# Kernel tuning notes

Measured on AMD Instinct MI355X. Metric: run time of the kernel, lower is better.

The kernel has to match this reference:

```python
import jax, jax.numpy as jnp
import numpy as np

H, N, CH, L = 256, 256, 1, 1024


def setup_inputs() -> dict:
    key = jax.random.key(0)
    k1, k2, k3, k4 = jax.random.split(key, 4)
    # Hurwitz-like A so the discretized dA is stable (|eig| < 1) over L powers
    A = 0.05 * jax.random.normal(k1, (H, N, N), jnp.float32) - jnp.eye(N, dtype=jnp.float32)
    B = jax.random.normal(k2, (H, N), jnp.float32)
    C = jax.random.normal(k3, (CH, H, N), jnp.float32)
    log_dt = jax.random.uniform(k4, (H,), jnp.float32,
                                minval=np.log(1e-3), maxval=np.log(1e-1))
    return {"A": A, "B": B, "C": C, "log_dt": log_dt}


def reference(A, B, C, log_dt):
    # Bilinear (Tustin) discretization:
    #   dA = (I - dt/2 A)^{-1} (I + dt/2 A),  dB = dt * (I - dt/2 A)^{-1} B
    dt = jnp.exp(log_dt)                                   # (H,)
    I = jnp.eye(A.shape[-1], dtype=A.dtype)
    A_bwd = I - (dt[:, None, None] / 2) * A                # (H, N, N)
    A_fwd = I + (dt[:, None, None] / 2) * A                # (H, N, N)
    dB = dt[:, None] * jnp.linalg.solve(A_bwd, B[..., None])[..., 0]   # (H, N)
    dA = jnp.linalg.solve(A_bwd, A_fwd)                    # (H, N, N)

    # Krylov kernel: k[c,h,l] = C[c,h,:] @ dA^l @ dB[h,:]
    def step(x, _):
        y = jnp.einsum('chn,hn->ch', C, x)                 # contract with C
        x_next = jnp.einsum('hmn,hn->hm', dA, x)           # advance state
        return x_next, y

    _, ys = jax.lax.scan(step, dB, None, length=L)         # ys: (L, CH, H)
    k = jnp.transpose(ys, (1, 2, 0))                       # (CH, H, L)
    return k
```

## Files before the change

### kernel.cpp

```cpp
#include <hip/hip_runtime.h>
#include <cstdint>
#include <cstddef>

#define NH 256
#define ND 256
#define NSV 32

typedef __attribute__((ext_vector_type(4))) float f32x4;
typedef __attribute__((ext_vector_type(8))) short short8;
typedef __attribute__((ext_vector_type(8))) unsigned short u16x8;
typedef __attribute__((ext_vector_type(4))) unsigned short u16x4;
typedef __attribute__((ext_vector_type(4))) unsigned int u32x4;

__device__ __forceinline__ float bfrec(unsigned short hi, unsigned short lo) {
  return __uint_as_float(((unsigned)hi) << 16) + __uint_as_float(((unsigned)lo) << 16);
}
__device__ __forceinline__ unsigned rne16(unsigned u) {
  return u + 0x7FFFu + ((u >> 16) & 1u);
}
__device__ __forceinline__ void bfsplit(float x, unsigned short& hi, unsigned short& lo) {
  unsigned u = __float_as_uint(x);
  unsigned r1 = rne16(u);
  hi = (unsigned short)(r1 >> 16);
  float lf = x - __uint_as_float(r1 & 0xFFFF0000u);
  unsigned r2 = rne16(__float_as_uint(lf));
  lo = (unsigned short)(r2 >> 16);
}
__device__ __forceinline__ void gload16(const void* g, void* l) {
  __builtin_amdgcn_global_load_lds(
      (const __attribute__((address_space(1))) unsigned int*)g,
      (__attribute__((address_space(3))) unsigned int*)l, 16, 0, 0);
}
__device__ __forceinline__ int ksw(int row) { return (row >> 1) & 3; }

__global__ __launch_bounds__(256) void prep_kernel(
    const float* __restrict__ A, const float* __restrict__ log_dt,
    unsigned short* __restrict__ Mhi, unsigned short* __restrict__ Mlo)
{
  size_t e0 = ((size_t)blockIdx.x * 256 + threadIdx.x) * 16;
  int h = (int)(e0 >> 16);
  float hdt = 0.5f * __expf(log_dt[h]);
  unsigned short hb[16], lb[16];
#pragma unroll
  for (int i = 0; i < 4; ++i) {
    f32x4 v = *(const f32x4*)(A + e0 + i * 4);
#pragma unroll
    for (int j = 0; j < 4; ++j) bfsplit(v[j] * hdt, hb[i * 4 + j], lb[i * 4 + j]);
  }
  unsigned ph[8], pl[8];
#pragma unroll
  for (int i = 0; i < 8; ++i) {
    ph[i] = (unsigned)hb[2 * i] | ((unsigned)hb[2 * i + 1] << 16);
    pl[i] = (unsigned)lb[2 * i] | ((unsigned)lb[2 * i + 1] << 16);
  }
  u32x4 a0 = {ph[0], ph[1], ph[2], ph[3]}, a1 = {ph[4], ph[5], ph[6], ph[7]};
  u32x4 b0 = {pl[0], pl[1], pl[2], pl[3]}, b1 = {pl[4], pl[5], pl[6], pl[7]};
  *(u32x4*)(Mhi + e0) = a0; *(u32x4*)(Mhi + e0 + 8) = a1;
  *(u32x4*)(Mlo + e0) = b0; *(u32x4*)(Mlo + e0 + 8) = b1;
}

template <int YI, int QOUT, int DBOUT>
__global__ __launch_bounds__(256) void gemm128_kernel(
    const unsigned short* __restrict__ Xhi, const unsigned short* __restrict__ Xlo,
    const unsigned short* __restrict__ Yhi, const unsigned short* __restrict__ Ylo,
    unsigned short* __restrict__ Dhi, unsigned short* __restrict__ Dlo,
    unsigned short* __restrict__ Qhi, unsigned short* __restrict__ Qlo,
    const float* __restrict__ Bv, float* __restrict__ dBraw)
{
  __shared__ unsigned short lds[33792];
  int tid = threadIdx.x;
  int lane = tid & 63, w = tid >> 6;
  int bid = blockIdx.x;
  int part = (bid >> 3) & 3;
  int h = ((bid >> 5) << 3) | (bid & 7);
  int m0 = (part >> 1) * 128, n0 = (part & 1) * 128;
  size_t mb = (size_t)h * 65536;

  f32x4 acc[2][8];
#pragma unroll
  for (int m = 0; m < 2; ++m)
#pragma unroll
    for (int n = 0; n < 8; ++n) { f32x4 z = {0.f, 0.f, 0.f, 0.f}; acc[m][n] = z; }

  auto STAGE = [&](int s, int kb) {
#pragma unroll
    for (int j = 0; j < 2; ++j) {
      int c = j * 256 + tid;
      {
        int row = c >> 2, sp = c & 3;
        size_t go = mb + (size_t)(m0 + row) * 256 + kb * 32 + ((sp ^ ksw(row)) << 3);
        gload16(Xhi + go, &lds[s * 8192 + c * 8]);
        gload16(Xlo + go, &lds[s * 8192 + 4096 + c * 8]);
      }
      {
        int k = c >> 4, ns = c & 15;
        size_t go = mb + (size_t)(kb * 32 + k) * 256 + n0 + ns * 8;
        gload16(Yhi + go, &lds[16384 + s * 8192 + c * 8]);
        gload16(Ylo + go, &lds[16384 + s * 8192 + 4096 + c * 8]);
      }
    }
  };

  STAGE(0, 0);
  __builtin_amdgcn_sched_barrier(0);

  int nn = tid & 127, kh = tid >> 7;
  int cur = 0;
  for (int kb = 0; kb < 8; ++kb) {
    int nxt = cur ^ 1;
    if (kb < 7) {
      STAGE(nxt, kb + 1);
      __builtin_amdgcn_sched_barrier(0);
      asm volatile("s_waitcnt vmcnt(8)" ::: "memory");
    } else {
      asm volatile("s_waitcnt vmcnt(0)" ::: "memory");
    }
    __builtin_amdgcn_sched_barrier(0);
    __builtin_amdgcn_s_barrier();
    __builtin_amdgcn_sched_barrier(0);

    unsigned short* yb = &lds[16384 + cur * 8192];
    unsigned short rh[16], rl[16];
#pragma unroll
    for (int i = 0; i < 16; ++i) {
      rh[i] = yb[(kh * 16 + i) * 128 + nn];
      rl[i] = yb[4096 + (kh * 16 + i) * 128 + nn];
    }
    asm volatile("s_waitcnt lgkmcnt(0)" ::: "memory");
    __builtin_amdgcn_sched_barrier(0);
    __builtin_amdgcn_s_barrier();
    __builtin_amdgcn_sched_barrier(0);

#pragma unroll
    for (int s2 = 0; s2 < 2; ++s2) {
      int sl = kh * 2 + s2;
      int off = nn * 32 + ((sl ^ ksw(nn)) << 3);
      u16x8 vh, vl;
#pragma unroll
      for (int e = 0; e < 8; ++e) {
        unsigned short hh = rh[s2 * 8 + e], ll = rl[s2 * 8 + e];
        if (YI) {
          if (kb * 32 + kh * 16 + s2 * 8 + e == n0 + nn) {
            float vv = bfrec(hh, ll) + 1.0f;
            bfsplit(vv, hh, ll);
          }
        }
        vh[e] = hh; vl[e] = ll;
      }
      *(u16x8*)&yb[off] = vh;
      *(u16x8*)&yb[4096 + off] = vl;
    }
    asm volatile("s_waitcnt lgkmcnt(0)" ::: "memory");
    __builtin_amdgcn_sched_barrier(0);
    __builtin_amdgcn_s_barrier();
    __builtin_amdgcn_sched_barrier(0);

    int kg = lane >> 4, li = lane & 15;
    const unsigned short* xb = &lds[cur * 8192];
    short8 bhi[8], blo[8];
#pragma unroll
    for (int n = 0; n < 8; ++n) {
      int rowN = n * 16 + li;
      int off = rowN * 32 + ((kg ^ ksw(rowN)) << 3);
      bhi[n] = *(const short8*)&yb[off];
      blo[n] = *(const short8*)&yb[4096 + off];
    }
    __builtin_amdgcn_s_setprio(1);
#pragma unroll
    for (int m = 0; m < 2; ++m) {
      int rowM = w * 32 + m * 16 + li;
      int off = rowM * 32 + ((kg ^ ksw(rowM)) << 3);
      short8 ahi = *(const short8*)&xb[off];
      short8 alo = *(const short8*)&xb[4096 + off];
#pragma unroll
      for (int n = 0; n < 8; ++n) {
        acc[m][n] = __builtin_amdgcn_mfma_f32_16x16x32_bf16(ahi, bhi[n], acc[m][n], 0, 0, 0);
        acc[m][n] = __builtin_amdgcn_mfma_f32_16x16x32_bf16(ahi, blo[n], acc[m][n], 0, 0, 0);
        acc[m][n] = __builtin_amdgcn_mfma_f32_16x16x32_bf16(alo, bhi[n], acc[m][n], 0, 0, 0);
      }
    }
    __builtin_amdgcn_s_setprio(0);
    __builtin_amdgcn_sched_barrier(0);
    __builtin_amdgcn_s_barrier();
    __builtin_amdgcn_sched_barrier(0);
    cur = nxt;
  }

  float* fb = (float*)lds;
  {
    int q0 = (lane >> 4) * 4, li = lane & 15;
#pragma unroll
    for (int m = 0; m < 2; ++m)
#pragma unroll
      for (int n = 0; n < 8; ++n)
#pragma unroll
        for (int q = 0; q < 4; ++q)
          fb[(w * 32 + m * 16 + q0 + q) * 132 + n * 16 + li] = acc[m][n][q];
  }
  __syncthreads();
  {
    int row = tid >> 1, half = tid & 1;
    float dacc = 0.f;
#pragma unroll 1
    for (int hp = 0; hp < 2; ++hp) {
      int c0 = half * 64 + hp * 32;
      float v[32];
#pragma unroll
      for (int u = 0; u < 8; ++u) {
        f32x4 t4 = *(const f32x4*)&fb[row * 132 + c0 + u * 4];
#pragma unroll
        for (int e = 0; e < 4; ++e) v[u * 4 + e] = t4[e];
      }
      size_t go = mb + (size_t)(m0 + row) * 256 + n0 + c0;
      if (DBOUT) {
        const float* Bp = Bv + h * 256 + n0 + c0;
#pragma unroll
        for (int u = 0; u < 8; ++u) {
          f32x4 b4 = *(const f32x4*)(Bp + u * 4);
#pragma unroll
          for (int e = 0; e < 4; ++e) dacc += v[u * 4 + e] * b4[e];
        }
      }
      {
        unsigned hw[16], lw[16];
#pragma unroll
        for (int i = 0; i < 16; ++i) {
          unsigned short ha, la, hb2, lb2;
          bfsplit(v[2 * i], ha, la);
          bfsplit(v[2 * i + 1], hb2, lb2);
          hw[i] = (unsigned)ha | ((unsigned)hb2 << 16);
          lw[i] = (unsigned)la | ((unsigned)lb2 << 16);
        }
#pragma unroll
        for (int u = 0; u < 4; ++u) {
          u32x4 a = {hw[u * 4], hw[u * 4 + 1], hw[u * 4 + 2], hw[u * 4 + 3]};
          u32x4 b = {lw[u * 4], lw[u * 4 + 1], lw[u * 4 + 2], lw[u * 4 + 3]};
          *(u32x4*)(Dhi + go + u * 8) = a;
          *(u32x4*)(Dlo + go + u * 8) = b;
        }
      }
      if (QOUT) {
        float xv[32];
#pragma unroll
        for (int u = 0; u < 4; ++u) {
          u16x8 xh = *(const u16x8*)(Xhi + go + u * 8);
          u16x8 xl = *(const u16x8*)(Xlo + go + u * 8);
#pragma unroll
          for (int e = 0; e < 8; ++e) xv[u * 8 + e] = bfrec(xh[e], xl[e]);
        }
        int grow = m0 + row, gc0 = n0 + c0;
        float qv[32];
#pragma unroll
        for (int e = 0; e < 32; ++e)
          qv[e] = v[e] + 2.f * xv[e] + ((gc0 + e) == grow ? 1.f : 0.f);
        unsigned hw[16], lw[16];
#pragma unroll
        for (int i = 0; i < 16; ++i) {
          unsigned short ha, la, hb2, lb2;
          bfsplit(qv[2 * i], ha, la);
          bfsplit(qv[2 * i + 1], hb2, lb2);
          hw[i] = (unsigned)ha | ((unsigned)hb2 << 16);
          lw[i] = (unsigned)la | ((unsigned)lb2 << 16);
        }
#pragma unroll
        for (int u = 0; u < 4; ++u) {
          u32x4 a = {hw[u * 4], hw[u * 4 + 1], hw[u * 4 + 2], hw[u * 4 + 3]};
          u32x4 b = {lw[u * 4], lw[u * 4 + 1], lw[u * 4 + 2], lw[u * 4 + 3]};
          *(u32x4*)(Qhi + go + u * 8) = a;
          *(u32x4*)(Qlo + go + u * 8) = b;
        }
      }
    }
    if (DBOUT) {
      int slab = (part & 1) * 2 + half;
      dBraw[(size_t)slab * 65536 + h * 256 + m0 + row] = dacc;
    }
  }
}

__device__ __forceinline__ int physc(int c) { return c + ((c >> 4) << 2); }

__global__ __launch_bounds__(1024, 4) void chain32_kernel(
    const unsigned short* __restrict__ dAhi, const unsigned short* __restrict__ dAlo,
    const unsigned short* __restrict__ Ghi, const unsigned short* __restrict__ Glo,
    const float* __restrict__ Cin, const float* __restrict__ Bv,
    const float* __restrict__ log_dt, const float* __restrict__ dBraw,
    float* __restrict__ U, float* __restrict__ W)
{
  int b = blockIdx.x;
  bool um = b < NH;
  int h = um ? b : b - NH;
  float* out = (um ? U : W) + (size_t)h * (NSV * 256);

  int tid = threadIdx.x;
  int rg = tid >> 4, cg = tid & 15;
  float mat[4][16];
  if (um) {
    const unsigned short* mh = dAhi + (size_t)h * 65536;
    const unsigned short* ml = dAlo + (size_t)h * 65536;
#pragma unroll
    for (int j = 0; j < 16; ++j) {
      u16x4 h4 = *(const u16x4*)(mh + (size_t)(cg * 16 + j) * 256 + rg * 4);
      u16x4 l4 = *(const u16x4*)(ml + (size_t)(cg * 16 + j) * 256 + rg * 4);
#pragma unroll
      for (int rr = 0; rr < 4; ++rr) mat[rr][j] = bfrec(h4[rr], l4[rr]);
    }
  } else {
    const unsigned short* mh = Ghi + (size_t)h * 65536;
    const unsigned short* ml = Glo + (size_t)h * 65536;
#pragma unroll
    for (int rr = 0; rr < 4; ++rr) {
      const unsigned short* ph = mh + (size_t)(rg * 4 + rr) * 256 + cg * 16;
      const unsigned short* pl = ml + (size_t)(rg * 4 + rr) * 256 + cg * 16;
      u16x8 h0 = *(const u16x8*)ph, h1 = *(const u16x8*)(ph + 8);
      u16x8 l0 = *(const u16x8*)pl, l1 = *(const u16x8*)(pl + 8);
#pragma unroll
      for (int e = 0; e < 8; ++e) {
        mat[rr][e] = bfrec(h0[e], l0[e]);
        mat[rr][8 + e] = bfrec(h1[e], l1[e]);
      }
    }
  }
  __shared__ float xb[2][320];
  __shared__ float slab[16][260];
  if (tid < 256) {
    float vv;
    if (um) {
      vv = Cin[(size_t)h * 256 + tid];
    } else {
      int o = h * 256 + tid;
      float raw = dBraw[o] + dBraw[65536 + o] + dBraw[131072 + o] + dBraw[196608 + o];
      vv = 0.5f * __expf(log_dt[h]) * (raw + Bv[o]);
    }
    xb[0][physc(tid)] = vv;
    out[tid] = vv;
  }
  __syncthreads();
  int p = 0;
  for (int v = 1; v < NSV; ++v) {
    f32x4 part = {0.f, 0.f, 0.f, 0.f};
#pragma unroll
    for (int sl = 0; sl < 4; ++sl) {
      f32x4 xv = *(const f32x4*)&xb[p][cg * 20 + sl * 4];
#pragma unroll
      for (int rr = 0; rr < 4; ++rr)
#pragma unroll
        for (int e = 0; e < 4; ++e) part[rr] += mat[rr][sl * 4 + e] * xv[e];
    }
    *(f32x4*)&slab[cg][rg * 4] = part;
    __syncthreads();
    if (tid < 256) {
      int row = tid;
      float s = 0.f;
#pragma unroll
      for (int c = 0; c < 16; ++c) s += slab[c][row];
      xb[p ^ 1][physc(row)] = s;
      out[(size_t)v * 256 + row] = s;
    }
    __syncthreads();
    p ^= 1;
  }
}

__global__ __launch_bounds__(512) void gram_kernel(
    const float* __restrict__ U, const float* __restrict__ W, float* __restrict__ out)
{
  int b = blockIdx.x;
  int h = b >> 1, jh = b & 1;
  __shared__ float ul[32][260];
  __shared__ float wl[16][260];
  int tid = threadIdx.x;
  const float* Up = U + (size_t)h * (NSV * 256);
  const float* Wp = W + (size_t)h * (NSV * 256) + (size_t)jh * 16 * 256;
  {
    int r = tid >> 4, cb = (tid & 15) * 16;
#pragma unroll
    for (int u = 0; u < 4; ++u) {
      f32x4 a = *(const f32x4*)(Up + (size_t)r * 256 + cb + u * 4);
      *(f32x4*)&ul[r][cb + u * 4] = a;
    }
  }
  {
    int r = tid >> 5, cb = (tid & 31) * 8;
    f32x4 a = *(const f32x4*)(Wp + (size_t)r * 256 + cb);
    f32x4 c2 = *(const f32x4*)(Wp + (size_t)r * 256 + cb + 4);
    *(f32x4*)&wl[r][cb] = a;
    *(f32x4*)&wl[r][cb + 4] = c2;
  }
  __syncthreads();
  int i = tid & 31, j2 = tid >> 5;
  float acc = 0.f;
#pragma unroll 8
  for (int c = 0; c < 256; c += 4) {
    f32x4 uu = *(const f32x4*)&ul[i][c];
    f32x4 ww = *(const f32x4*)&wl[j2][c];
    acc += uu[0] * ww[0] + uu[1] * ww[1] + uu[2] * ww[2] + uu[3] * ww[3];
  }
  out[(size_t)h * 1024 + (size_t)(jh * 16 + j2) * 32 + i] = acc;
}

__global__ void bail_kernel(float* out, unsigned mib) {
  if (threadIdx.x == 0) out[blockIdx.x] = -(2.0e6f + (float)mib * 4096.0f);
}

extern "C" void kernel_launch(void* const* d_in, const int* in_sizes, int n_in,
                              void* d_out, int out_size, void* d_ws, size_t ws_size,
                              hipStream_t stream) {
  const float* A = (const float*)d_in[0];
  const float* B = (const float*)d_in[1];
  const float* C = (const float*)d_in[2];
  const float* log_dt = (const float*)d_in[3];
  float* out = (float*)d_out;

  const size_t PLANE = (size_t)NH * ND * ND * 2;
  const size_t DBRAW = 4 * (size_t)NH * ND * 4;
  const size_t USZ = (size_t)NH * NSV * ND * 4;
  const size_t WSZ = USZ;
  const size_t NEED = 6 * PLANE + DBRAW + USZ + WSZ;
  if (ws_size < NEED) {
    bail_kernel<<<8, 64, 0, stream>>>(out, (unsigned)(ws_size >> 20));
    return;
  }
  uint8_t* w8 = (uint8_t*)d_ws;
  auto P = [&](int i) -> unsigned short* { return (unsigned short*)(w8 + (size_t)i * PLANE); };
  float* dBraw = (float*)(w8 + 6 * PLANE);
  float* Up = (float*)(w8 + 6 * PLANE + DBRAW);
  float* Wp = (float*)(w8 + 6 * PLANE + DBRAW + USZ);

  prep_kernel<<<4096, 256, 0, stream>>>(A, log_dt, P(0), P(1));
  gemm128_kernel<0, 1, 0><<<1024, 256, 0, stream>>>(P(0), P(1), P(0), P(1),
                                                    P(2), P(3), P(4), P(5), nullptr, nullptr);
  gemm128_kernel<1, 0, 0><<<1024, 256, 0, stream>>>(P(4), P(5), P(2), P(3),
                                                    P(0), P(1), nullptr, nullptr, nullptr, nullptr);
  gemm128_kernel<0, 0, 0><<<1024, 256, 0, stream>>>(P(2), P(3), P(2), P(3),
                                                    P(4), P(5), nullptr, nullptr, nullptr, nullptr);
  gemm128_kernel<1, 0, 1><<<1024, 256, 0, stream>>>(P(0), P(1), P(4), P(5),
                                                    P(2), P(3), nullptr, nullptr, B, dBraw);
  gemm128_kernel<0, 0, 0><<<1024, 256, 0, stream>>>(P(2), P(3), P(2), P(3),
                                                    P(0), P(1), nullptr, nullptr, nullptr, nullptr);
  gemm128_kernel<0, 0, 0><<<1024, 256, 0, stream>>>(P(0), P(1), P(0), P(1),
                                                    P(4), P(5), nullptr, nullptr, nullptr, nullptr);
  gemm128_kernel<0, 0, 0><<<1024, 256, 0, stream>>>(P(4), P(5), P(4), P(5),
                                                    P(0), P(1), nullptr, nullptr, nullptr, nullptr);
  gemm128_kernel<0, 0, 0><<<1024, 256, 0, stream>>>(P(0), P(1), P(0), P(1),
                                                    P(4), P(5), nullptr, nullptr, nullptr, nullptr);
  gemm128_kernel<0, 0, 0><<<1024, 256, 0, stream>>>(P(4), P(5), P(4), P(5),
                                                    P(0), P(1), nullptr, nullptr, nullptr, nullptr);
  chain32_kernel<<<2 * NH, 1024, 0, stream>>>(P(2), P(3), P(0), P(1),
                                              C, B, log_dt, dBraw, Up, Wp);
  gram_kernel<<<2 * NH, 512, 0, stream>>>(Up, Wp, out);
}
```

Measured before the change: 585.9 us.

## Use 512-thread blocks for 128x128 GEMM tiles with separate transposed-B LDS buffer

Doubles the GEMM workgroup from 256 to 512 threads so each wave computes a 16-row slice instead of 32, halving per-thread accumulators, staging loads and epilogue work. The B-transpose now writes to a dedicated LDS region, which removes one barrier per k-step. The epilogue splits each row across four threads, and the dB partial-sum slabs grow from 4 to 8, with the chain kernel summing all 8. The aim is more waves to hide latency, at the cost of more LDS per block, a 4-waves-per-SIMD register cap, and more dBraw workspace.

```diff
diff --git a/kernel.cpp b/kernel.cpp
--- a/kernel.cpp
+++ b/kernel.cpp
@@ -60,14 +60,14 @@
 }
 
 template <int YI, int QOUT, int DBOUT>
-__global__ __launch_bounds__(256) void gemm128_kernel(
+__global__ __launch_bounds__(512, 4) void gemm128_kernel(
     const unsigned short* __restrict__ Xhi, const unsigned short* __restrict__ Xlo,
     const unsigned short* __restrict__ Yhi, const unsigned short* __restrict__ Ylo,
     unsigned short* __restrict__ Dhi, unsigned short* __restrict__ Dlo,
     unsigned short* __restrict__ Qhi, unsigned short* __restrict__ Qlo,
     const float* __restrict__ Bv, float* __restrict__ dBraw)
 {
-  __shared__ unsigned short lds[33792];
+  __shared__ unsigned short lds[40960];
   int tid = threadIdx.x;
   int lane = tid & 63, w = tid >> 6;
   int bid = blockIdx.x;
@@ -76,28 +76,22 @@
   int m0 = (part >> 1) * 128, n0 = (part & 1) * 128;
   size_t mb = (size_t)h * 65536;
 
-  f32x4 acc[2][8];
-#pragma unroll
-  for (int m = 0; m < 2; ++m)
-#pragma unroll
-    for (int n = 0; n < 8; ++n) { f32x4 z = {0.f, 0.f, 0.f, 0.f}; acc[m][n] = z; }
+  f32x4 acc[8];
+#pragma unroll
+  for (int n = 0; n < 8; ++n) { f32x4 z = {0.f, 0.f, 0.f, 0.f}; acc[n] = z; }
 
   auto STAGE = [&](int s, int kb) {
-#pragma unroll
-    for (int j = 0; j < 2; ++j) {
-      int c = j * 256 + tid;
-      {
-        int row = c >> 2, sp = c & 3;
-        size_t go = mb + (size_t)(m0 + row) * 256 + kb * 32 + ((sp ^ ksw(row)) << 3);
-        gload16(Xhi + go, &lds[s * 8192 + c * 8]);
-        gload16(Xlo + go, &lds[s * 8192 + 4096 + c * 8]);
-      }
-      {
-        int k = c >> 4, ns = c & 15;
-        size_t go = mb + (size_t)(kb * 32 + k) * 256 + n0 + ns * 8;
-        gload16(Yhi + go, &lds[16384 + s * 8192 + c * 8]);
-        gload16(Ylo + go, &lds[16384 + s * 8192 + 4096 + c * 8]);
-      }
+    {
+      int row = tid >> 2, sp = tid & 3;
+      size_t go = mb + (size_t)(m0 + row) * 256 + kb * 32 + ((sp ^ ksw(row)) << 3);
+      gload16(Xhi + go, &lds[s * 8192 + tid * 8]);
+      gload16(Xlo + go, &lds[s * 8192 + 4096 + tid * 8]);
+    }
+    {
+      int k = tid >> 4, ns = tid & 15;
+      size_t go = mb + (size_t)(kb * 32 + k) * 256 + n0 + ns * 8;
+      gload16(Yhi + go, &lds[16384 + s * 8192 + tid * 8]);
+      gload16(Ylo + go, &lds[16384 + s * 8192 + 4096 + tid * 8]);
     }
   };
 
@@ -111,7 +105,7 @@
     if (kb < 7) {
       STAGE(nxt, kb + 1);
       __builtin_amdgcn_sched_barrier(0);
-      asm volatile("s_waitcnt vmcnt(8)" ::: "memory");
+      asm volatile("s_waitcnt vmcnt(4)" ::: "memory");
     } else {
       asm volatile("s_waitcnt vmcnt(0)" ::: "memory");
     }
@@ -119,67 +113,59 @@
     __builtin_amdgcn_s_barrier();
     __builtin_amdgcn_sched_barrier(0);
 
-    unsigned short* yb = &lds[16384 + cur * 8192];
-    unsigned short rh[16], rl[16];
-#pragma unroll
-    for (int i = 0; i < 16; ++i) {
-      rh[i] = yb[(kh * 16 + i) * 128 + nn];
-      rl[i] = yb[4096 + (kh * 16 + i) * 128 + nn];
-    }
-    asm volatile("s_waitcnt lgkmcnt(0)" ::: "memory");
-    __builtin_amdgcn_sched_barrier(0);
-    __builtin_amdgcn_s_barrier();
-    __builtin_amdgcn_sched_barrier(0);
-
-#pragma unroll
-    for (int s2 = 0; s2 < 2; ++s2) {
-      int sl = kh * 2 + s2;
-      int off = nn * 32 + ((sl ^ ksw(nn)) << 3);
+    {
+      const unsigned short* yb = &lds[16384 + cur * 8192];
+      unsigned short rh[8], rl[8];
+#pragma unroll
+      for (int i = 0; i < 8; ++i) {
+        rh[i] = yb[(kh * 8 + i) * 128 + nn];
+        rl[i] = yb[4096 + (kh * 8 + i) * 128 + nn];
+      }
+      int off = nn * 32 + ((kh ^ ksw(nn)) << 3);
       u16x8 vh, vl;
 #pragma unroll
       for (int e = 0; e < 8; ++e) {
-        unsigned short hh = rh[s2 * 8 + e], ll = rl[s2 * 8 + e];
+        unsigned short hh = rh[e], ll = rl[e];
         if (YI) {
-          if (kb * 32 + kh * 16 + s2 * 8 + e == n0 + nn) {
+          if (kb * 32 + kh * 8 + e == n0 + nn) {
             float vv = bfrec(hh, ll) + 1.0f;
             bfsplit(vv, hh, ll);
           }
         }
         vh[e] = hh; vl[e] = ll;
       }
-      *(u16x8*)&yb[off] = vh;
-      *(u16x8*)&yb[4096 + off] = vl;
+      *(u16x8*)&lds[32768 + off] = vh;
+      *(u16x8*)&lds[36864 + off] = vl;
     }
     asm volatile("s_waitcnt lgkmcnt(0)" ::: "memory");
     __builtin_amdgcn_sched_barrier(0);
     __builtin_amdgcn_s_barrier();
     __builtin_amdgcn_sched_barrier(0);
 
-    int kg = lane >> 4, li = lane & 15;
-    const unsigned short* xb = &lds[cur * 8192];
-    short8 bhi[8], blo[8];
-#pragma unroll
-    for (int n = 0; n < 8; ++n) {
-      int rowN = n * 16 + li;
-      int off = rowN * 32 + ((kg ^ ksw(rowN)) << 3);
-      bhi[n] = *(const short8*)&yb[off];
-      blo[n] = *(const short8*)&yb[4096 + off];
-    }
-    __builtin_amdgcn_s_setprio(1);
-#pragma unroll
-    for (int m = 0; m < 2; ++m) {
-      int rowM = w * 32 + m * 16 + li;
-      int off = rowM * 32 + ((kg ^ ksw(rowM)) << 3);
-      short8 ahi = *(const short8*)&xb[off];
-      short8 alo = *(const short8*)&xb[4096 + off];
+    {
+      int kg = lane >> 4, li = lane & 15;
+      const unsigned short* xb = &lds[cur * 8192];
+      short8 bhi[8], blo[8];
 #pragma unroll
       for (int n = 0; n < 8; ++n) {
-        acc[m][n] = __builtin_amdgcn_mfma_f32_16x16x32_bf16(ahi, bhi[n], acc[m][n], 0, 0, 0);
-        acc[m][n] = __builtin_amdgcn_mfma_f32_16x16x32_bf16(ahi, blo[n], acc[m][n], 0, 0, 0);
-        acc[m][n] = __builtin_amdgcn_mfma_f32_16x16x32_bf16(alo, bhi[n], acc[m][n], 0, 0, 0);
-      }
-    }
-    __builtin_amdgcn_s_setprio(0);
+        int rowN = n * 16 + li;
+        int off = rowN * 32 + ((kg ^ ksw(rowN)) << 3);
+        bhi[n] = *(const short8*)&lds[32768 + off];
+        blo[n] = *(const short8*)&lds[36864 + off];
+      }
+      int rowM = w * 16 + li;
+      int offm = rowM * 32 + ((kg ^ ksw(rowM)) << 3);
+      short8 ahi = *(const short8*)&xb[offm];
+      short8 alo = *(const short8*)&xb[4096 + offm];
+      __builtin_amdgcn_s_setprio(1);
+#pragma unroll
+      for (int n = 0; n < 8; ++n) {
+        acc[n] = __builtin_amdgcn_mfma_f32_16x16x32_bf16(ahi, bhi[n], acc[n], 0, 0, 0);
+        acc[n] = __builtin_amdgcn_mfma_f32_16x16x32_bf16(ahi, blo[n], acc[n], 0, 0, 0);
+        acc[n] = __builtin_amdgcn_mfma_f32_16x16x32_bf16(alo, bhi[n], acc[n], 0, 0, 0);
+      }
+      __builtin_amdgcn_s_setprio(0);
+    }
     __builtin_amdgcn_sched_barrier(0);
     __builtin_amdgcn_s_barrier();
     __builtin_amdgcn_sched_barrier(0);
@@ -190,89 +176,84 @@
   {
     int q0 = (lane >> 4) * 4, li = lane & 15;
 #pragma unroll
-    for (int m = 0; m < 2; ++m)
-#pragma unroll
-      for (int n = 0; n < 8; ++n)
-#pragma unroll
-        for (int q = 0; q < 4; ++q)
-          fb[(w * 32 + m * 16 + q0 + q) * 132 + n * 16 + li] = acc[m][n][q];
+    for (int n = 0; n < 8; ++n)
+#pragma unroll
+      for (int q = 0; q < 4; ++q)
+        fb[(w * 16 + q0 + q) * 132 + n * 16 + li] = acc[n][q];
   }
   __syncthreads();
   {
-    int row = tid >> 1, half = tid & 1;
+    int row = tid >> 2, qc = tid & 3, c0 = qc * 32;
+    float v[32];
+#pragma unroll
+    for (int uu = 0; uu < 8; ++uu) {
+      int u = (uu + qc * 2) & 7;
+      f32x4 t4 = *(const f32x4*)&fb[row * 132 + c0 + u * 4];
+#pragma unroll
+      for (int e = 0; e < 4; ++e) v[u * 4 + e] = t4[e];
+    }
+    size_t go = mb + (size_t)(m0 + row) * 256 + n0 + c0;
     float dacc = 0.f;
-#pragma unroll 1
-    for (int hp = 0; hp < 2; ++hp) {
-      int c0 = half * 64 + hp * 32;
-      float v[32];
+    if (DBOUT) {
+      const float* Bp = Bv + h * 256 + n0 + c0;
 #pragma unroll
       for (int u = 0; u < 8; ++u) {
-        f32x4 t4 = *(const f32x4*)&fb[row * 132 + c0 + u * 4];
-#pragma unroll
-        for (int e = 0; e < 4; ++e) v[u * 4 + e] = t4[e];
-      }
-      size_t go = mb + (size_t)(m0 + row) * 256 + n0 + c0;
-      if (DBOUT) {
-        const float* Bp = Bv + h * 256 + n0 + c0;
-#pragma unroll
-        for (int u = 0; u < 8; ++u) {
-          f32x4 b4 = *(const f32x4*)(Bp + u * 4);
-#pragma unroll
-          for (int e = 0; e < 4; ++e) dacc += v[u * 4 + e] * b4[e];
-        }
-      }
-      {
-        unsigned hw[16], lw[16];
-#pragma unroll
-        for (int i = 0; i < 16; ++i) {
-          unsigned short ha, la, hb2, lb2;
-          bfsplit(v[2 * i], ha, la);
-          bfsplit(v[2 * i + 1], hb2, lb2);
-          hw[i] = (unsigned)ha | ((unsigned)hb2 << 16);
-          lw[i] = (unsigned)la | ((unsigned)lb2 << 16);
-        }
-#pragma unroll
-        for (int u = 0; u < 4; ++u) {
-          u32x4 a = {hw[u * 4], hw[u * 4 + 1], hw[u * 4 + 2], hw[u * 4 + 3]};
-          u32x4 b = {lw[u * 4], lw[u * 4 + 1], lw[u * 4 + 2], lw[u * 4 + 3]};
-          *(u32x4*)(Dhi + go + u * 8) = a;
-          *(u32x4*)(Dlo + go + u * 8) = b;
-        }
-      }
-      if (QOUT) {
-        float xv[32];
-#pragma unroll
-        for (int u = 0; u < 4; ++u) {
-          u16x8 xh = *(const u16x8*)(Xhi + go + u * 8);
-          u16x8 xl = *(const u16x8*)(Xlo + go + u * 8);
-#pragma unroll
-          for (int e = 0; e < 8; ++e) xv[u * 8 + e] = bfrec(xh[e], xl[e]);
-        }
-        int grow = m0 + row, gc0 = n0 + c0;
-        float qv[32];
-#pragma unroll
-        for (int e = 0; e < 32; ++e)
-          qv[e] = v[e] + 2.f * xv[e] + ((gc0 + e) == grow ? 1.f : 0.f);
-        unsigned hw[16], lw[16];
-#pragma unroll
-        for (int i = 0; i < 16; ++i) {
-          unsigned short ha, la, hb2, lb2;
-          bfsplit(qv[2 * i], ha, la);
-          bfsplit(qv[2 * i + 1], hb2, lb2);
-          hw[i] = (unsigned)ha | ((unsigned)hb2 << 16);
-          lw[i] = (unsigned)la | ((unsigned)lb2 << 16);
-        }
-#pragma unroll
-        for (int u = 0; u < 4; ++u) {
-          u32x4 a = {hw[u * 4], hw[u * 4 + 1], hw[u * 4 + 2], hw[u * 4 + 3]};
-          u32x4 b = {lw[u * 4], lw[u * 4 + 1], lw[u * 4 + 2], lw[u * 4 + 3]};
-          *(u32x4*)(Qhi + go + u * 8) = a;
-          *(u32x4*)(Qlo + go + u * 8) = b;
-        }
+        f32x4 b4 = *(const f32x4*)(Bp + u * 4);
+#pragma unroll
+        for (int e = 0; e < 4; ++e) dacc += v[u * 4 + e] * b4[e];
+      }
+    }
+    {
+      unsigned hw[16], lw[16];
+#pragma unroll
+      for (int i = 0; i < 16; ++i) {
+        unsigned short ha, la, hb2, lb2;
+        bfsplit(v[2 * i], ha, la);
+        bfsplit(v[2 * i + 1], hb2, lb2);
+        hw[i] = (unsigned)ha | ((unsigned)hb2 << 16);
+        lw[i] = (unsigned)la | ((unsigned)lb2 << 16);
+      }
+#pragma unroll
+      for (int u = 0; u < 4; ++u) {
+        u32x4 a = {hw[u * 4], hw[u * 4 + 1], hw[u * 4 + 2], hw[u * 4 + 3]};
+        u32x4 b = {lw[u * 4], lw[u * 4 + 1], lw[u * 4 + 2], lw[u * 4 + 3]};
+        *(u32x4*)(Dhi + go + u * 8) = a;
+        *(u32x4*)(Dlo + go + u * 8) = b;
+      }
+    }
+    if (QOUT) {
+      float xv[32];
+#pragma unroll
+      for (int u = 0; u < 4; ++u) {
+        u16x8 xh = *(const u16x8*)(Xhi + go + u * 8);
+        u16x8 xl = *(const u16x8*)(Xlo + go + u * 8);
+#pragma unroll
+        for (int e = 0; e < 8; ++e) xv[u * 8 + e] = bfrec(xh[e], xl[e]);
+      }
+      int grow = m0 + row, gc0 = n0 + c0;
+      float qv[32];
+#pragma unroll
+      for (int e = 0; e < 32; ++e)
+        qv[e] = v[e] + 2.f * xv[e] + ((gc0 + e) == grow ? 1.f : 0.f);
+      unsigned hw[16], lw[16];
+#pragma unroll
+      for (int i = 0; i < 16; ++i) {
+        unsigned short ha, la, hb2, lb2;
+        bfsplit(qv[2 * i], ha, la);
+        bfsplit(qv[2 * i + 1], hb2, lb2);
+        hw[i] = (unsigned)ha | ((unsigned)hb2 << 16);
+        lw[i] = (unsigned)la | ((unsigned)lb2 << 16);
+      }
+#pragma unroll
+      for (int u = 0; u < 4; ++u) {
+        u32x4 a = {hw[u * 4], hw[u * 4 + 1], hw[u * 4 + 2], hw[u * 4 + 3]};
+        u32x4 b = {lw[u * 4], lw[u * 4 + 1], lw[u * 4 + 2], lw[u * 4 + 3]};
+        *(u32x4*)(Qhi + go + u * 8) = a;
+        *(u32x4*)(Qlo + go + u * 8) = b;
       }
     }
     if (DBOUT) {
-      int slab = (part & 1) * 2 + half;
+      int slab = (part & 1) * 4 + qc;
       dBraw[(size_t)slab * 65536 + h * 256 + m0 + row] = dacc;
     }
   }
@@ -329,7 +310,9 @@
       vv = Cin[(size_t)h * 256 + tid];
     } else {
       int o = h * 256 + tid;
-      float raw = dBraw[o] + dBraw[65536 + o] + dBraw[131072 + o] + dBraw[196608 + o];
+      float raw = 0.f;
+#pragma unroll
+      for (int s = 0; s < 8; ++s) raw += dBraw[(size_t)s * 65536 + o];
       vv = 0.5f * __expf(log_dt[h]) * (raw + Bv[o]);
     }
     xb[0][physc(tid)] = vv;
@@ -413,7 +396,7 @@
   float* out = (float*)d_out;
 
   const size_t PLANE = (size_t)NH * ND * ND * 2;
-  const size_t DBRAW = 4 * (size_t)NH * ND * 4;
+  const size_t DBRAW = 8 * (size_t)NH * ND * 4;
   const size_t USZ = (size_t)NH * NSV * ND * 4;
   const size_t WSZ = USZ;
   const size_t NEED = 6 * PLANE + DBRAW + USZ + WSZ;
@@ -428,23 +411,23 @@
   float* Wp = (float*)(w8 + 6 * PLANE + DBRAW + USZ);
 
   prep_kernel<<<4096, 256, 0, stream>>>(A, log_dt, P(0), P(1));
-  gemm128_kernel<0, 1, 0><<<1024, 256, 0, stream>>>(P(0), P(1), P(0), P(1),
+  gemm128_kernel<0, 1, 0><<<1024, 512, 0, stream>>>(P(0), P(1), P(0), P(1),
                                                     P(2), P(3), P(4), P(5), nullptr, nullptr);
-  gemm128_kernel<1, 0, 0><<<1024, 256, 0, stream>>>(P(4), P(5), P(2), P(3),
+  gemm128_kernel<1, 0, 0><<<1024, 512, 0, stream>>>(P(4), P(5), P(2), P(3),
                                                     P(0), P(1), nullptr, nullptr, nullptr, nullptr);
-  gemm128_kernel<0, 0, 0><<<1024, 256, 0, stream>>>(P(2), P(3), P(2), P(3),
+  gemm128_kernel<0, 0, 0><<<1024, 512, 0, stream>>>(P(2), P(3), P(2), P(3),
                                                     P(4), P(5), nullptr, nullptr, nullptr, nullptr);
-  gemm128_kernel<1, 0, 1><<<1024, 256, 0, stream>>>(P(0), P(1), P(4), P(5),
+  gemm128_kernel<1, 0, 1><<<1024, 512, 0, stream>>>(P(0), P(1), P(4), P(5),
                                                     P(2), P(3), nullptr, nullptr, B, dBraw);
-  gemm128_kernel<0, 0, 0><<<1024, 256, 0, stream>>>(P(2), P(3), P(2), P(3),
+  gemm128_kernel<0, 0, 0><<<1024, 512, 0, stream>>>(P(2), P(3), P(2), P(3),
                                                     P(0), P(1), nullptr, nullptr, nullptr, nullptr);
-  gemm128_kernel<0, 0, 0><<<1024, 256, 0, stream>>>(P(0), P(1), P(0), P(1),
+  gemm128_kernel<0, 0, 0><<<1024, 512, 0, stream>>>(P(0), P(1), P(0), P(1),
                                                     P(4), P(5), nullptr, nullptr, nullptr, nullptr);
-  gemm128_kernel<0, 0, 0><<<1024, 256, 0, stream>>>(P(4), P(5), P(4), P(5),
+  gemm128_kernel<0, 0, 0><<<1024, 512, 0, stream>>>(P(4), P(5), P(4), P(5),
                                                     P(0), P(1), nullptr, nullptr, nullptr, nullptr);
-  gemm128_kernel<0, 0, 0><<<1024, 256, 0, stream>>>(P(0), P(1), P(0), P(1),
+  gemm128_kernel<0, 0, 0><<<1024, 512, 0, stream>>>(P(0), P(1), P(0), P(1),
                                                     P(4), P(5), nullptr, nullptr, nullptr, nullptr);
-  gemm128_kernel<0, 0, 0><<<1024, 256, 0, stream>>>(P(4), P(5), P(4), P(5),
+  gemm128_kernel<0, 0, 0><<<1024, 512, 0, stream>>>(P(4), P(5), P(4), P(5),
                                                     P(0), P(1), nullptr, nullptr, nullptr, nullptr);
   chain32_kernel<<<2 * NH, 1024, 0, stream>>>(P(2), P(3), P(0), P(1),
                                               C, B, log_dt, dBraw, Up, Wp);
```

Result: slower. 1.001 ms (+70.9%).
